# Optimization experiments

Measured on AMD Instinct MI355X. Metric: run time of the kernel, lower is better.

## Reference

```python
import jax, jax.numpy as jnp
import numpy as np


def setup_inputs() -> dict:
    key = jax.random.key(0)
    ks = jax.random.split(key, 5)
    B, T, C, es = 32, 2048, 256, 256
    stdv = 1.0 / np.sqrt(es)
    return {
        "x": jax.random.normal(ks[0], (B, T, C), dtype=jnp.float32),
        "h0": jnp.zeros((B, es), dtype=jnp.float32),
        "c0": jnp.zeros((B, es), dtype=jnp.float32),
        "W1": jax.random.uniform(ks[1], (C, 4 * es), minval=-stdv, maxval=stdv, dtype=jnp.float32),
        "W2": jax.random.uniform(ks[2], (es, 4 * es), minval=-stdv, maxval=stdv, dtype=jnp.float32),
        "b1": jax.random.uniform(ks[3], (4 * es,), minval=-stdv, maxval=stdv, dtype=jnp.float32),
        "b2": jax.random.uniform(ks[4], (4 * es,), minval=-stdv, maxval=stdv, dtype=jnp.float32),
    }


def reference(x, h0, c0, W1, W2, b1, b2):
    B, T, C = x.shape
    es = W2.shape[0]
    # input-side gate preactivations for all timesteps at once: [T, B, 4*es]
    pre = jnp.transpose(jnp.einsum("btc,cg->btg", x, W1) + b1 + b2, (1, 0, 2))

    def step(carry, pre_t):
        h, c = carry
        v = pre_t + h @ W2  # [B, 4*es]
        f = jax.nn.sigmoid(v[:, :es])
        i = jax.nn.sigmoid(v[:, es:2 * es])
        o = jax.nn.sigmoid(v[:, 2 * es:3 * es])
        c_hat = jnp.tanh(v[:, 3 * es:])
        c_new = f * c + i * c_hat
        h_new = o * jnp.tanh(c_new)
        return (h_new, c_new), h_new

    (h, c), out_h_2 = jax.lax.scan(step, (h0, c0), pre)  # out_h_2: [T, B, es]
    # torch.cat(out_h, dim=-1): [B, T*es]
    out_h_1 = jnp.transpose(out_h_2, (1, 0, 2)).reshape(B, T * es)
    return (out_h_1, out_h_2, (h, c))
```

## Files before the change

kernel.cpp:

```cpp
#include <hip/hip_runtime.h>

typedef unsigned int u32;
typedef unsigned short u16;
typedef unsigned long long u64;
typedef __attribute__((ext_vector_type(2))) _Float16 h2v;
typedef __attribute__((ext_vector_type(4))) _Float16 f16x4;
typedef __attribute__((ext_vector_type(4))) float f32x4;

#define BB 32
#define TT 2048
#define CC 256
#define ESZ 256
#define GG 1024
#define NG 4
#define NW 128

__device__ __forceinline__ float fdot2u(u32 a, u32 b, float c) {
#if __has_builtin(__builtin_amdgcn_fdot2)
  return __builtin_amdgcn_fdot2(__builtin_bit_cast(h2v, a), __builtin_bit_cast(h2v, b), c, false);
#else
  h2v av = __builtin_bit_cast(h2v, a), bv = __builtin_bit_cast(h2v, b);
  return c + (float)av[0] * (float)bv[0] + (float)av[1] * (float)bv[1];
#endif
}

__device__ __forceinline__ float sigm_f(float x) {
  float e = __builtin_amdgcn_exp2f(x * -1.442695041f);
  return __builtin_amdgcn_rcpf(1.0f + e);
}
__device__ __forceinline__ float tanh_f(float x) {
  float e = __builtin_amdgcn_exp2f(x * 2.885390082f);
  return 1.0f - 2.0f * __builtin_amdgcn_rcpf(e + 1.0f);
}

__global__ void k_pack_w2(const float* __restrict__ W2, u32* __restrict__ W2p) {
  int gid = blockIdx.x * 256 + threadIdx.x;
  int m = gid >> 10, j = gid & 1023;
  _Float16 lo = (_Float16)W2[(size_t)(2 * m) * GG + j];
  _Float16 hi = (_Float16)W2[(size_t)(2 * m + 1) * GG + j];
  W2p[gid] = (u32)__builtin_bit_cast(u16, lo) | ((u32)__builtin_bit_cast(u16, hi) << 16);
}

__global__ void k_init_slab(const float* __restrict__ h0, u64* __restrict__ slab) {
  int idx = blockIdx.x * 256 + threadIdx.x;
  int slot = idx >> 12;
  int rem = idx & 4095;
  int b = rem >> 7, r = rem & 127;
  u64 word = 0;
  if (slot == 0) {
    _Float16 lo = (_Float16)h0[b * ESZ + 2 * r];
    _Float16 hi = (_Float16)h0[b * ESZ + 2 * r + 1];
    u32 h2 = (u32)__builtin_bit_cast(u16, lo) | ((u32)__builtin_bit_cast(u16, hi) << 16);
    word = ((u64)h2 << 32);
  }
  slab[(size_t)slot * (BB * NW) + b * NW + r] = word;
}

__global__ __launch_bounds__(256, 2) void k_pre_gemm(
    const float* __restrict__ x, const float* __restrict__ W1,
    const float* __restrict__ b1, const float* __restrict__ b2,
    _Float16* __restrict__ pre) {
  __shared__ __attribute__((aligned(16))) _Float16 Al[128 * 36];
  __shared__ __attribute__((aligned(16))) _Float16 Bl[64 * 36];
  const int tid = threadIdx.x;
  const int lane = tid & 63, wv = tid >> 6;
  const int wr = wv >> 1, wc = wv & 1;
  const int rowBase = blockIdx.x * 128;
  const int colBase = blockIdx.y * 64;

  f32x4 acc[4][2];
#pragma unroll
  for (int mi = 0; mi < 4; ++mi)
#pragma unroll
    for (int ni = 0; ni < 2; ++ni) acc[mi][ni] = (f32x4){0.f, 0.f, 0.f, 0.f};

  for (int k0 = 0; k0 < 256; k0 += 32) {
#pragma unroll
    for (int i = 0; i < 4; ++i) {
      int fidx = tid + 256 * i;
      int row = fidx >> 3, kc = (fidx & 7) * 4;
      const float4 v = *(const float4*)(x + (size_t)(rowBase + row) * 256 + k0 + kc);
      f16x4 hv = { (_Float16)v.x, (_Float16)v.y, (_Float16)v.z, (_Float16)v.w };
      *(f16x4*)&Al[row * 36 + kc] = hv;
    }
#pragma unroll
    for (int i = 0; i < 8; ++i) {
      int idx = tid + 256 * i;
      int k = idx >> 6, n = idx & 63;
      Bl[n * 36 + k] = (_Float16)W1[(size_t)(k0 + k) * GG + colBase + n];
    }
    __syncthreads();

#pragma unroll
    for (int kk = 0; kk < 2; ++kk) {
      int ka = (lane >> 4) * 4 + kk * 16;
      f16x4 af[4], bf[2];
#pragma unroll
      for (int mi = 0; mi < 4; ++mi)
        af[mi] = *(const f16x4*)&Al[(wr * 64 + mi * 16 + (lane & 15)) * 36 + ka];
#pragma unroll
      for (int ni = 0; ni < 2; ++ni)
        bf[ni] = *(const f16x4*)&Bl[(wc * 32 + ni * 16 + (lane & 15)) * 36 + ka];
#pragma unroll
      for (int mi = 0; mi < 4; ++mi)
#pragma unroll
        for (int ni = 0; ni < 2; ++ni)
          acc[mi][ni] = __builtin_amdgcn_mfma_f32_16x16x16f16(af[mi], bf[ni], acc[mi][ni], 0, 0, 0);
    }
    __syncthreads();
  }

#pragma unroll
  for (int ni = 0; ni < 2; ++ni) {
    int col = colBase + wc * 32 + ni * 16 + (lane & 15);
    float bias = b1[col] + b2[col];
#pragma unroll
    for (int mi = 0; mi < 4; ++mi) {
      int r0 = rowBase + wr * 64 + mi * 16 + (lane >> 4) * 4;
#pragma unroll
      for (int rr = 0; rr < 4; ++rr)
        pre[(size_t)(r0 + rr) * GG + col] = (_Float16)(acc[mi][ni][rr] + bias);
    }
  }
}

__global__ __launch_bounds__(256, 1)
__attribute__((amdgpu_waves_per_eu(1, 1)))
void k_lstm_rec(
    const _Float16* __restrict__ pre, const u32* __restrict__ W2p,
    const float* __restrict__ c0, u64* __restrict__ slab,
    float* __restrict__ out1, float* __restrict__ out2,
    float* __restrict__ hN, float* __restrict__ cN) {
  const int bid = blockIdx.x;
  const int b = bid & 31;
  const int g = bid >> 5;
  const int t = threadIdx.x;
  const int l = t & 63;
  const int w = t >> 6;
  const int es_l = l & 15;
  const int gate = l >> 4;
  const int E0 = 64 * g + 16 * w;
  const int j = E0 + es_l;
  const int col = j + 256 * gate;

  u32 wreg[128];
#pragma unroll
  for (int m = 0; m < 128; ++m) wreg[m] = W2p[m * GG + col];

  float creg = c0[b * ESZ + j];

  const _Float16* preB = pre + (size_t)b * TT * GG;
  _Float16 q = preB[col];

  const int rA = l;
  const int rB = 64 + l;
  float hv_keep = 0.f;

  for (int s = 0; s < TT; ++s) {
    u64* basep = slab + (size_t)(s & 1) * (BB * NW) + b * NW;
    u64 wA, wB;
    u32 want = (u32)s;
    do {
      wA = __hip_atomic_load(&basep[rA], __ATOMIC_RELAXED, __HIP_MEMORY_SCOPE_AGENT);
    } while ((u32)wA != want);
    do {
      wB = __hip_atomic_load(&basep[rB], __ATOMIC_RELAXED, __HIP_MEMORY_SCOPE_AGENT);
    } while ((u32)wB != want);
    u32 hvA = (u32)(wA >> 32);
    u32 hvB = (u32)(wB >> 32);

    float A0 = 0.f, A1 = 0.f, A2 = 0.f, A3 = 0.f;
    float qf = (float)q;
    if (s + 1 < TT) q = preB[(size_t)(s + 1) * GG + col];

#pragma unroll
    for (int m = 0; m < 32; ++m) {
      u32 h0m = (u32)__builtin_amdgcn_readlane((int)hvA, m);
      u32 h1m = (u32)__builtin_amdgcn_readlane((int)hvA, 32 + m);
      u32 h2m = (u32)__builtin_amdgcn_readlane((int)hvB, m);
      u32 h3m = (u32)__builtin_amdgcn_readlane((int)hvB, 32 + m);
      A0 = fdot2u(h0m, wreg[m], A0);
      A1 = fdot2u(h1m, wreg[32 + m], A1);
      A2 = fdot2u(h2m, wreg[64 + m], A2);
      A3 = fdot2u(h3m, wreg[96 + m], A3);
    }
    float v = qf + ((A0 + A1) + (A2 + A3));
    float gv = (gate == 3) ? tanh_f(v) : sigm_f(v);

    float fg = __shfl(gv, es_l);
    float ig = __shfl(gv, es_l + 16);
    float og = __shfl(gv, es_l + 32);
    float ch = __shfl(gv, es_l + 48);
    creg = fg * creg + ig * ch;
    float hv = og * tanh_f(creg);
    hv_keep = hv;

    if (l < 16) {
      out1[(size_t)b * TT * ESZ + (size_t)s * ESZ + j] = hv;
      out2[(size_t)s * (BB * ESZ) + b * ESZ + j] = hv;
    }

    float hp = __shfl_xor(hv, 1);
    if (l < 16 && (es_l & 1) == 0) {
      _Float16 lo16 = (_Float16)hv, hi16 = (_Float16)hp;
      u32 h2p = (u32)__builtin_bit_cast(u16, lo16) | ((u32)__builtin_bit_cast(u16, hi16) << 16);
      u64 word = ((u64)h2p << 32) | (u32)(s + 1);
      int r = (E0 + es_l) >> 1;
      u64* outp = slab + (size_t)((s + 1) & 1) * (BB * NW) + b * NW + r;
      __hip_atomic_store(outp, word, __ATOMIC_RELAXED, __HIP_MEMORY_SCOPE_AGENT);
    }
  }

  if (l < 16) {
    hN[b * ESZ + j] = hv_keep;
    cN[b * ESZ + j] = creg;
  }
}

extern "C" void kernel_launch(void* const* d_in, const int* in_sizes, int n_in,
                              void* d_out, int out_size, void* d_ws, size_t ws_size,
                              hipStream_t stream) {
  const float* x  = (const float*)d_in[0];
  const float* h0 = (const float*)d_in[1];
  const float* c0 = (const float*)d_in[2];
  const float* W1 = (const float*)d_in[3];
  const float* W2 = (const float*)d_in[4];
  const float* b1 = (const float*)d_in[5];
  const float* b2 = (const float*)d_in[6];

  float* out1 = (float*)d_out;
  float* out2 = out1 + (size_t)BB * TT * ESZ;
  float* hN   = out2 + (size_t)BB * TT * ESZ;
  float* cN   = hN + BB * ESZ;

  _Float16* pre = (_Float16*)d_ws;
  u32* W2p = (u32*)((char*)d_ws + (size_t)BB * TT * GG * 2);
  u64* slab = (u64*)((char*)W2p + 128 * GG * 4);

  k_pack_w2<<<512, 256, 0, stream>>>(W2, W2p);
  k_init_slab<<<32, 256, 0, stream>>>(h0, slab);
  k_pre_gemm<<<dim3(512, 16), 256, 0, stream>>>(x, W1, b1, b2, pre);

  k_lstm_rec<<<NG * BB, 256, 0, stream>>>(pre, W2p, c0, slab, out1, out2, hN, cN);
}
```

Before: 3.517 ms.

## Split recurrent K dimension across wave pairs and double the block count

The recurrent step is reorganized so each wave handles half of the hidden-state reduction (64 packed weights instead of 128), with pairs of waves combining partial sums through double-buffered shared memory and a block barrier. The grid doubles to 256 blocks, so each block covers 32 hidden units instead of 64. The aim is to shorten the serial per-step dot-product chain and spread work over more CUs. The cost is an extra intra-block barrier and LDS exchange every timestep, plus more blocks polling the global slab.

```diff
diff --git a/kernel.cpp b/kernel.cpp
--- a/kernel.cpp
+++ b/kernel.cpp
@@ -12,7 +12,7 @@
 #define CC 256
 #define ESZ 256
 #define GG 1024
-#define NG 4
+#define NG 8
 #define NW 128
 
 __device__ __forceinline__ float fdot2u(u32 a, u32 b, float c) {
@@ -131,88 +131,92 @@
     const float* __restrict__ c0, u64* __restrict__ slab,
     float* __restrict__ out1, float* __restrict__ out2,
     float* __restrict__ hN, float* __restrict__ cN) {
+  __shared__ float part[2][4][64];
+
   const int bid = blockIdx.x;
   const int b = bid & 31;
   const int g = bid >> 5;
   const int t = threadIdx.x;
   const int l = t & 63;
   const int w = t >> 6;
+  const int half = w & 1;
+  const int set = w >> 1;
   const int es_l = l & 15;
   const int gate = l >> 4;
-  const int E0 = 64 * g + 16 * w;
+  const int E0 = 32 * g + 16 * set;
   const int j = E0 + es_l;
   const int col = j + 256 * gate;
 
-  u32 wreg[128];
-#pragma unroll
-  for (int m = 0; m < 128; ++m) wreg[m] = W2p[m * GG + col];
-
-  float creg = c0[b * ESZ + j];
+  u32 wreg[64];
+#pragma unroll
+  for (int m = 0; m < 64; ++m) wreg[m] = W2p[(64 * half + m) * GG + col];
+
+  float creg = 0.f, hlast = 0.f;
+  if (!half) creg = c0[b * ESZ + j];
 
   const _Float16* preB = pre + (size_t)b * TT * GG;
-  _Float16 q = preB[col];
-
-  const int rA = l;
-  const int rB = 64 + l;
-  float hv_keep = 0.f;
+  _Float16 q = (_Float16)0.f;
+  if (!half) q = preB[col];
 
   for (int s = 0; s < TT; ++s) {
-    u64* basep = slab + (size_t)(s & 1) * (BB * NW) + b * NW;
-    u64 wA, wB;
-    u32 want = (u32)s;
+    u64* basep = slab + (size_t)(s & 1) * (BB * NW) + b * NW + 64 * half;
+    u64 wv_;
     do {
-      wA = __hip_atomic_load(&basep[rA], __ATOMIC_RELAXED, __HIP_MEMORY_SCOPE_AGENT);
-    } while ((u32)wA != want);
-    do {
-      wB = __hip_atomic_load(&basep[rB], __ATOMIC_RELAXED, __HIP_MEMORY_SCOPE_AGENT);
-    } while ((u32)wB != want);
-    u32 hvA = (u32)(wA >> 32);
-    u32 hvB = (u32)(wB >> 32);
-
-    float A0 = 0.f, A1 = 0.f, A2 = 0.f, A3 = 0.f;
-    float qf = (float)q;
-    if (s + 1 < TT) q = preB[(size_t)(s + 1) * GG + col];
-
-#pragma unroll
-    for (int m = 0; m < 32; ++m) {
-      u32 h0m = (u32)__builtin_amdgcn_readlane((int)hvA, m);
-      u32 h1m = (u32)__builtin_amdgcn_readlane((int)hvA, 32 + m);
-      u32 h2m = (u32)__builtin_amdgcn_readlane((int)hvB, m);
-      u32 h3m = (u32)__builtin_amdgcn_readlane((int)hvB, 32 + m);
-      A0 = fdot2u(h0m, wreg[m], A0);
-      A1 = fdot2u(h1m, wreg[32 + m], A1);
-      A2 = fdot2u(h2m, wreg[64 + m], A2);
-      A3 = fdot2u(h3m, wreg[96 + m], A3);
-    }
-    float v = qf + ((A0 + A1) + (A2 + A3));
-    float gv = (gate == 3) ? tanh_f(v) : sigm_f(v);
-
-    float fg = __shfl(gv, es_l);
-    float ig = __shfl(gv, es_l + 16);
-    float og = __shfl(gv, es_l + 32);
-    float ch = __shfl(gv, es_l + 48);
-    creg = fg * creg + ig * ch;
-    float hv = og * tanh_f(creg);
-    hv_keep = hv;
-
-    if (l < 16) {
-      out1[(size_t)b * TT * ESZ + (size_t)s * ESZ + j] = hv;
-      out2[(size_t)s * (BB * ESZ) + b * ESZ + j] = hv;
-    }
-
-    float hp = __shfl_xor(hv, 1);
-    if (l < 16 && (es_l & 1) == 0) {
-      _Float16 lo16 = (_Float16)hv, hi16 = (_Float16)hp;
-      u32 h2p = (u32)__builtin_bit_cast(u16, lo16) | ((u32)__builtin_bit_cast(u16, hi16) << 16);
-      u64 word = ((u64)h2p << 32) | (u32)(s + 1);
-      int r = (E0 + es_l) >> 1;
-      u64* outp = slab + (size_t)((s + 1) & 1) * (BB * NW) + b * NW + r;
-      __hip_atomic_store(outp, word, __ATOMIC_RELAXED, __HIP_MEMORY_SCOPE_AGENT);
-    }
-  }
-
-  if (l < 16) {
-    hN[b * ESZ + j] = hv_keep;
+      wv_ = __hip_atomic_load(&basep[l], __ATOMIC_RELAXED, __HIP_MEMORY_SCOPE_AGENT);
+    } while ((u32)wv_ != (u32)s);
+    u32 hv_ = (u32)(wv_ >> 32);
+
+    float A0 = 0.f, A1 = 0.f;
+#pragma unroll
+    for (int k = 0; k < 32; ++k) {
+      u32 hm0 = (u32)__builtin_amdgcn_readlane((int)hv_, 2 * k);
+      u32 hm1 = (u32)__builtin_amdgcn_readlane((int)hv_, 2 * k + 1);
+      A0 = fdot2u(hm0, wreg[2 * k], A0);
+      A1 = fdot2u(hm1, wreg[2 * k + 1], A1);
+    }
+    float A = A0 + A1;
+
+    float qf = 0.f;
+    if (!half) {
+      qf = (float)q;
+      if (s + 1 < TT) q = preB[(size_t)(s + 1) * GG + col];
+    } else {
+      part[s & 1][w][l] = A;
+    }
+
+    asm volatile("s_waitcnt lgkmcnt(0)" ::: "memory");
+    __builtin_amdgcn_s_barrier();
+
+    if (!half) {
+      float v = A + qf + part[s & 1][w | 1][l];
+      float gv = (gate == 3) ? tanh_f(v) : sigm_f(v);
+
+      float fg = __shfl(gv, es_l);
+      float ig = __shfl(gv, es_l + 16);
+      float og = __shfl(gv, es_l + 32);
+      float ch = __shfl(gv, es_l + 48);
+      creg = fg * creg + ig * ch;
+      float hv = og * tanh_f(creg);
+      hlast = hv;
+
+      float hp = __shfl_xor(hv, 1);
+      if (l < 16 && (l & 1) == 0) {
+        _Float16 lo16 = (_Float16)hv, hi16 = (_Float16)hp;
+        u32 h2p = (u32)__builtin_bit_cast(u16, lo16) | ((u32)__builtin_bit_cast(u16, hi16) << 16);
+        u64 word = ((u64)h2p << 32) | (u32)(s + 1);
+        int r = (E0 + l) >> 1;
+        u64* outp = slab + (size_t)((s + 1) & 1) * (BB * NW) + b * NW + r;
+        __hip_atomic_store(outp, word, __ATOMIC_RELAXED, __HIP_MEMORY_SCOPE_AGENT);
+      }
+      if (l < 16) {
+        out1[(size_t)b * TT * ESZ + (size_t)s * ESZ + j] = hv;
+        out2[(size_t)s * (BB * ESZ) + b * ESZ + j] = hv;
+      }
+    }
+  }
+
+  if (!half && l < 16) {
+    hN[b * ESZ + j] = hlast;
     cN[b * ESZ + j] = creg;
   }
 }
```

Measured after the change: 3.267 ms. 1.08x faster.
